# Optimization experiments

Measured on AMD Instinct MI355X. Metric: run time of the kernel, lower is better.

Reference implementation:

```python
import jax, jax.numpy as jnp
import numpy as np

WINDOW_SIZE = 7
NUM_HEADS = 6
DIM = 192
HEAD_DIM = DIM // NUM_HEADS


def _relative_position_index(ws: int) -> np.ndarray:
    coords = np.stack(np.meshgrid(np.arange(ws), np.arange(ws), indexing='ij'))  # [2, ws, ws]
    coords = coords.reshape(2, -1)  # [2, ws*ws]
    rel = coords[:, :, None] - coords[:, None, :]  # [2, N, N]
    rel = rel.transpose(1, 2, 0).astype(np.int64)  # [N, N, 2]
    rel[..., 0] += ws - 1
    rel[..., 1] += ws - 1
    rel[..., 0] *= 2 * ws - 1
    return rel.sum(-1)  # [N, N] in [0, (2*ws-1)^2)


def setup_inputs() -> dict:
    key = jax.random.key(0)
    ks = jax.random.split(key, 6)
    B, N, C = 8192, WINDOW_SIZE * WINDOW_SIZE, DIM
    return {
        'x': jax.random.normal(ks[0], (B, N, C), dtype=jnp.float32),
        'qkv_w': jax.random.normal(ks[1], (3 * C, C), dtype=jnp.float32) * 0.02,
        'qkv_b': jax.random.normal(ks[2], (3 * C,), dtype=jnp.float32) * 0.02,
        'proj_w': jax.random.normal(ks[3], (C, C), dtype=jnp.float32) * 0.02,
        'proj_b': jax.random.normal(ks[4], (C,), dtype=jnp.float32) * 0.02,
        'bias_table': jax.random.normal(ks[5], ((2 * WINDOW_SIZE - 1) ** 2, NUM_HEADS), dtype=jnp.float32) * 0.02,
    }


def reference(x, qkv_w, qkv_b, proj_w, proj_b, bias_table):
    B, N, C = x.shape
    H, hd = NUM_HEADS, HEAD_DIM
    scale = hd ** -0.5
    rel_idx = jnp.asarray(_relative_position_index(WINDOW_SIZE))  # [N, N] static

    qkv = x @ qkv_w.T + qkv_b  # [B, N, 3C]
    qkv = qkv.reshape(B, N, 3, H, hd).transpose(2, 0, 3, 1, 4)  # [3, B, H, N, hd]
    q, k, v = qkv[0], qkv[1], qkv[2]

    attn = jnp.einsum('bhnd,bhmd->bhnm', q * scale, k)  # [B, H, N, N]
    bias = bias_table[rel_idx]  # [N, N, H]
    attn = attn + bias.transpose(2, 0, 1)[None]  # broadcast over B
    attn = jax.nn.softmax(attn, axis=-1)

    out = jnp.einsum('bhnm,bhmd->bhnd', attn, v)  # [B, H, N, hd]
    out = out.transpose(0, 2, 1, 3).reshape(B, N, C)
    return out @ proj_w.T + proj_b
```

## Files before the change

kernel.cpp:

```cpp
#include <hip/hip_runtime.h>
#include <hip/hip_bf16.h>
#include <cstdint>
#include <cstddef>

typedef float  f32x4 __attribute__((ext_vector_type(4)));
typedef short  s16x8 __attribute__((ext_vector_type(8)));

#define NTOK   49
#define CDIM   192
#define HEADS  6
#define SCALE  0.17677669529663689f
#define LOG2E  1.4426950408889634f
#define SCL2   (0.17677669529663689f * 1.4426950408889634f)

#define WS_BIAS_BYTES  98304
#define WS_WQ_BYTES    221184
#define WS_TOTAL_BYTES (WS_BIAS_BYTES + WS_WQ_BYTES + 73728)

static __device__ __forceinline__ ushort f2bf(float f) {
  __hip_bfloat16 h = __float2bfloat16(f);
  union { __hip_bfloat16 h; ushort u; } c; c.h = h;
  return c.u;
}

static __device__ __forceinline__ s16x8 pack8(f32x4 a, f32x4 b) {
  union { s16x8 v; __hip_bfloat162 h[4]; } u;
  u.h[0] = __float22bfloat162_rn(make_float2(a[0], a[1]));
  u.h[1] = __float22bfloat162_rn(make_float2(a[2], a[3]));
  u.h[2] = __float22bfloat162_rn(make_float2(b[0], b[1]));
  u.h[3] = __float22bfloat162_rn(make_float2(b[2], b[3]));
  return u.v;
}

static __device__ __forceinline__ f32x4 mfma_bf16(s16x8 a, s16x8 b, f32x4 c) {
  return __builtin_amdgcn_mfma_f32_16x16x32_bf16(a, b, c, 0, 0, 0);
}

__global__ void wconv_kernel(const float* __restrict__ qkv_w,
                             const float* __restrict__ proj_w,
                             const float* __restrict__ bias_table,
                             ushort* __restrict__ wqs, ushort* __restrict__ wps,
                             float* __restrict__ biasT) {
  int i = blockIdx.x * 256 + threadIdx.x;
  if (i < 576 * 192) {
    int n = i / 192, k = i % 192;
    int dst = ((n >> 4) * 6 + (k >> 5)) * 512 + ((k >> 3) & 3) * 128 + (n & 15) * 8 + (k & 7);
    wqs[dst] = f2bf(qkv_w[i]);
  }
  if (i < 192 * 192) {
    int n = i / 192, k = i % 192;
    int dst = ((n >> 4) * 6 + (k >> 5)) * 512 + ((k >> 3) & 3) * 128 + (n & 15) * 8 + (k & 7);
    wps[dst] = f2bf(proj_w[i]);
  }
  if (i < HEADS * 4096) {
    int h = i >> 12, r = i & 4095;
    int lane = (r >> 2) & 63, e = r & 3;
    int qt = r >> 10, kt = (r >> 8) & 3;
    int q   = qt * 16 + (lane & 15);
    int key = kt * 16 + (lane >> 4) * 4 + e;
    float v;
    if (key >= NTOK)      v = -1e30f;
    else if (q >= NTOK)   v = 0.f;
    else {
      int qd = q / 7, qm = q % 7, kd = key / 7, km = key % 7;
      int ri = (qd - kd + 6) * 13 + (qm - km + 6);
      v = bias_table[ri * 6 + h] * LOG2E;
    }
    biasT[i] = v;
  }
}

template <bool WB>
__global__ __launch_bounds__(768, 3)
void wattn_kernel(const float* __restrict__ x,
                  const float* __restrict__ qkv_w, const float* __restrict__ qkv_b,
                  const float* __restrict__ proj_w, const float* __restrict__ proj_b,
                  const float* __restrict__ bias_table,
                  const ushort* __restrict__ wqs, const ushort* __restrict__ wps,
                  const float* __restrict__ biasT,
                  float* __restrict__ out, int nwin) {
  __shared__ __align__(16) ushort XB[2][64 * 200];
  __shared__ __align__(16) float  BL[WB ? 4 : 1024];

  const int tid  = threadIdx.x;
  const int lane = tid & 63;
  const int wv   = tid >> 6;
  const int winl = wv / 6;
  const int w    = wv - winl * 6;
  const int l16  = lane & 15;
  const int lk   = lane >> 4;
  const int win  = blockIdx.x * 2 + winl;
  const int h    = w;

#pragma unroll
  for (int it = 0; it < 8; ++it) {
    int v = tid + it * 768;
    int wl2 = v / 3072, r = v - wl2 * 3072;
    int row = r / 48, c4 = r - row * 48;
    int wgl = blockIdx.x * 2 + wl2;
    float4 f = {0.f, 0.f, 0.f, 0.f};
    if (row < NTOK && wgl < nwin)
      f = *(const float4*)(x + (size_t)wgl * (NTOK * CDIM) + row * CDIM + c4 * 4);
    union { ushort4 u; __hip_bfloat162 h[2]; } cc;
    cc.h[0] = __float22bfloat162_rn(make_float2(f.x, f.y));
    cc.h[1] = __float22bfloat162_rn(make_float2(f.z, f.w));
    *(ushort4*)&XB[wl2][row * 200 + c4 * 4] = cc.u;
  }
  if constexpr (!WB) {
    for (int v = tid; v < 169 * 6; v += 768) BL[v] = bias_table[v];
  }
  __syncthreads();

  s16x8 bq[4], ak[4], bv[2][2];

  {
    f32x4 qacc[2][4] = {};
    f32x4 kacc[2][4] = {};
#pragma unroll
    for (int ks = 0; ks < 6; ++ks) {
      const int k0 = ks * 32 + lk * 8;
      s16x8 xa[4];
#pragma unroll
      for (int mt = 0; mt < 4; ++mt)
        xa[mt] = *(const s16x8*)&XB[winl][(mt * 16 + l16) * 200 + k0];
#pragma unroll
      for (int nt2 = 0; nt2 < 2; ++nt2) {
        s16x8 wqf, wkf;
        if constexpr (WB) {
          const int lo = lk * 128 + l16 * 8;
          wqf = *(const s16x8*)&wqs[(((0 * 12 + w * 2 + nt2) * 6 + ks) << 9) + lo];
          wkf = *(const s16x8*)&wqs[(((1 * 12 + w * 2 + nt2) * 6 + ks) << 9) + lo];
        } else {
          const int nq = w * 32 + nt2 * 16 + l16;
          const float* p;
          p = qkv_w + (0 * 192 + nq) * 192 + k0;
          { float4 f0 = *(const float4*)p, f1 = *(const float4*)(p + 4);
            f32x4 a = {f0.x,f0.y,f0.z,f0.w}, b = {f1.x,f1.y,f1.z,f1.w}; wqf = pack8(a, b); }
          p = qkv_w + (1 * 192 + nq) * 192 + k0;
          { float4 f0 = *(const float4*)p, f1 = *(const float4*)(p + 4);
            f32x4 a = {f0.x,f0.y,f0.z,f0.w}, b = {f1.x,f1.y,f1.z,f1.w}; wkf = pack8(a, b); }
        }
#pragma unroll
        for (int mt = 0; mt < 4; ++mt) {
          qacc[nt2][mt] = mfma_bf16(wqf, xa[mt], qacc[nt2][mt]);
          kacc[nt2][mt] = mfma_bf16(wkf, xa[mt], kacc[nt2][mt]);
        }
      }
    }
    {
      const float4 b0 = *(const float4*)&qkv_b[0 * 192 + w * 32 +  0 + lk * 4];
      const float4 b1 = *(const float4*)&qkv_b[0 * 192 + w * 32 + 16 + lk * 4];
#pragma unroll
      for (int t = 0; t < 4; ++t) {
        f32x4 a0 = qacc[0][t], a1 = qacc[1][t];
        a0[0]=(a0[0]+b0.x)*SCL2; a0[1]=(a0[1]+b0.y)*SCL2; a0[2]=(a0[2]+b0.z)*SCL2; a0[3]=(a0[3]+b0.w)*SCL2;
        a1[0]=(a1[0]+b1.x)*SCL2; a1[1]=(a1[1]+b1.y)*SCL2; a1[2]=(a1[2]+b1.z)*SCL2; a1[3]=(a1[3]+b1.w)*SCL2;
        bq[t] = pack8(a0, a1);
      }
    }
#pragma unroll
    for (int t = 0; t < 4; ++t)
      ak[t] = pack8(kacc[0][t], kacc[1][t]);
  }

  {
    f32x4 vacc[4][2] = {};
#pragma unroll
    for (int ks = 0; ks < 6; ++ks) {
      const int k0 = ks * 32 + lk * 8;
      s16x8 xa[4];
#pragma unroll
      for (int mt = 0; mt < 4; ++mt)
        xa[mt] = *(const s16x8*)&XB[winl][(mt * 16 + l16) * 200 + k0];
#pragma unroll
      for (int nt2 = 0; nt2 < 2; ++nt2) {
        s16x8 wf;
        if constexpr (WB) {
          wf = *(const s16x8*)&wqs[(((2 * 12 + w * 2 + nt2) * 6 + ks) << 9) + lk * 128 + l16 * 8];
        } else {
          const float* p = qkv_w + (2 * 192 + w * 32 + nt2 * 16 + l16) * 192 + k0;
          float4 f0 = *(const float4*)p, f1 = *(const float4*)(p + 4);
          f32x4 a = {f0.x,f0.y,f0.z,f0.w}, b = {f1.x,f1.y,f1.z,f1.w}; wf = pack8(a, b);
        }
#pragma unroll
        for (int mt = 0; mt < 4; ++mt)
          vacc[mt][nt2] = mfma_bf16(xa[mt], wf, vacc[mt][nt2]);
      }
    }
#pragma unroll
    for (int nd = 0; nd < 2; ++nd) {
      const float vb = qkv_b[2 * 192 + w * 32 + nd * 16 + l16];
      f32x4 v0 = vacc[0][nd], v1 = vacc[1][nd], v2 = vacc[2][nd], v3 = vacc[3][nd];
#pragma unroll
      for (int i = 0; i < 4; ++i) { v0[i]+=vb; v1[i]+=vb; v2[i]+=vb; v3[i]+=vb; }
      bv[nd][0] = pack8(v0, v1);
      bv[nd][1] = pack8(v2, v3);
    }
  }
  __syncthreads();

#pragma unroll
  for (int qt = 0; qt < 4; ++qt) {
    f32x4 s[4];
#pragma unroll
    for (int kt = 0; kt < 4; ++kt) {
      f32x4 z = {0.f, 0.f, 0.f, 0.f};
      s[kt] = mfma_bf16(ak[kt], bq[qt], z);
    }
    float mx = -1e30f;
    if constexpr (WB) {
#pragma unroll
      for (int kt = 0; kt < 4; ++kt) {
        f32x4 b4 = *(const f32x4*)&biasT[h * 4096 + qt * 1024 + kt * 256 + lane * 4];
#pragma unroll
        for (int i = 0; i < 4; ++i) {
          float sv = s[kt][i] + b4[i];
          s[kt][i] = sv;
          mx = fmaxf(mx, sv);
        }
      }
    } else {
      const int q  = qt * 16 + l16;
      const int qd = q / 7, qm = q % 7;
#pragma unroll
      for (int kt = 0; kt < 4; ++kt)
#pragma unroll
        for (int i = 0; i < 4; ++i) {
          const int key = kt * 16 + lk * 4 + i;
          float sv = s[kt][i];
          if (key < NTOK) {
            int kd = key / 7, km = key % 7;
            int ri = (qd - kd + 6) * 13 + (qm - km + 6);
            ri = ri < 0 ? 0 : (ri > 168 ? 168 : ri);
            sv += BL[ri * 6 + h] * LOG2E;
          } else sv = -1e30f;
          s[kt][i] = sv;
          mx = fmaxf(mx, sv);
        }
    }
    mx = fmaxf(mx, __shfl_xor(mx, 16));
    mx = fmaxf(mx, __shfl_xor(mx, 32));
    float sum = 0.f;
#pragma unroll
    for (int kt = 0; kt < 4; ++kt)
#pragma unroll
      for (int i = 0; i < 4; ++i) {
        float p = exp2f(s[kt][i] - mx);
        s[kt][i] = p; sum += p;
      }
    sum += __shfl_xor(sum, 16);
    sum += __shfl_xor(sum, 32);
    const float rinv = 1.f / sum;
#pragma unroll
    for (int kt = 0; kt < 4; ++kt)
#pragma unroll
      for (int i = 0; i < 4; ++i) s[kt][i] *= rinv;

    s16x8 pa0 = pack8(s[0], s[1]);
    s16x8 pa1 = pack8(s[2], s[3]);
#pragma unroll
    for (int nd = 0; nd < 2; ++nd) {
      f32x4 z = {0.f, 0.f, 0.f, 0.f};
      f32x4 o = mfma_bf16(pa0, bv[nd][0], z);
      o = mfma_bf16(pa1, bv[nd][1], o);
#pragma unroll
      for (int i = 0; i < 4; ++i)
        XB[winl][(qt * 16 + lk * 4 + i) * 200 + h * 32 + nd * 16 + l16] = f2bf(o[i]);
    }
  }
  __syncthreads();

  {
    f32x4 pc[4][2] = {};
#pragma unroll
    for (int ks = 0; ks < 6; ++ks) {
      const int k0 = ks * 32 + lk * 8;
      s16x8 a[4];
#pragma unroll
      for (int mt = 0; mt < 4; ++mt)
        a[mt] = *(const s16x8*)&XB[winl][(mt * 16 + l16) * 200 + k0];
#pragma unroll
      for (int nt = 0; nt < 2; ++nt) {
        s16x8 b;
        if constexpr (WB) {
          b = *(const s16x8*)&wps[(((w * 2 + nt) * 6 + ks) << 9) + lk * 128 + l16 * 8];
        } else {
          const int n = w * 32 + nt * 16 + l16;
          const float* p = proj_w + n * 192 + k0;
          float4 f0 = *(const float4*)p, f1 = *(const float4*)(p + 4);
          f32x4 fa = {f0.x,f0.y,f0.z,f0.w}, fb = {f1.x,f1.y,f1.z,f1.w};
          b = pack8(fa, fb);
        }
#pragma unroll
        for (int mt = 0; mt < 4; ++mt)
          pc[mt][nt] = mfma_bf16(a[mt], b, pc[mt][nt]);
      }
    }
    if (win < nwin) {
#pragma unroll
      for (int nt = 0; nt < 2; ++nt) {
        const int n = w * 32 + nt * 16 + l16;
        const float pbias = proj_b[n];
#pragma unroll
        for (int mt = 0; mt < 4; ++mt)
#pragma unroll
          for (int i = 0; i < 4; ++i) {
            const int row = mt * 16 + lk * 4 + i;
            if (row < NTOK)
              out[((size_t)win * NTOK + row) * CDIM + n] = pc[mt][nt][i] + pbias;
          }
      }
    }
  }
}

extern "C" void kernel_launch(void* const* d_in, const int* in_sizes, int n_in,
                              void* d_out, int out_size, void* d_ws, size_t ws_size,
                              hipStream_t stream) {
  const float* x          = (const float*)d_in[0];
  const float* qkv_w      = (const float*)d_in[1];
  const float* qkv_b      = (const float*)d_in[2];
  const float* proj_w     = (const float*)d_in[3];
  const float* proj_b     = (const float*)d_in[4];
  const float* bias_table = (const float*)d_in[5];
  float* out = (float*)d_out;

  const int nwin = in_sizes[0] / (NTOK * CDIM);
  const int nblk = (nwin + 1) / 2;

  if (ws_size >= WS_TOTAL_BYTES) {
    float*  biasT = (float*)d_ws;
    ushort* wqs   = (ushort*)((char*)d_ws + WS_BIAS_BYTES);
    ushort* wps   = (ushort*)((char*)d_ws + WS_BIAS_BYTES + WS_WQ_BYTES);
    wconv_kernel<<<dim3(432), dim3(256), 0, stream>>>(qkv_w, proj_w, bias_table, wqs, wps, biasT);
    wattn_kernel<true><<<dim3(nblk), dim3(768), 0, stream>>>(
        x, qkv_w, qkv_b, proj_w, proj_b, bias_table, wqs, wps, biasT, out, nwin);
  } else {
    wattn_kernel<false><<<dim3(nblk), dim3(768), 0, stream>>>(
        x, qkv_w, qkv_b, proj_w, proj_b, bias_table, nullptr, nullptr, nullptr, out, nwin);
  }
}
```

Baseline: 409.0 us.

## Make attention blocks persistent over four window pairs with double-buffered x prefetch

Each block now processes four window pairs in a loop instead of one, using a double-buffered LDS region. The global loads of the next pair's x are issued into registers before the attention phase and written to the alternate buffer afterward, so load latency overlaps compute and launch count drops by four. In exchange it doubles LDS use per block (about 100KB), which may cut occupancy below the launch-bounds target, and adds register pressure from the staged float4s. Grid size shrinks, so tail and load-balance effects change.

```diff
diff --git a/kernel.cpp b/kernel.cpp
--- a/kernel.cpp
+++ b/kernel.cpp
@@ -12,6 +12,7 @@
 #define SCALE  0.17677669529663689f
 #define LOG2E  1.4426950408889634f
 #define SCL2   (0.17677669529663689f * 1.4426950408889634f)
+#define PPB    4
 
 #define WS_BIAS_BYTES  98304
 #define WS_WQ_BYTES    221184
@@ -21,6 +22,13 @@
   __hip_bfloat16 h = __float2bfloat16(f);
   union { __hip_bfloat16 h; ushort u; } c; c.h = h;
   return c.u;
+}
+
+static __device__ __forceinline__ ushort4 cvt4(float4 f) {
+  union { ushort4 u; __hip_bfloat162 h[2]; } cc;
+  cc.h[0] = __float22bfloat162_rn(make_float2(f.x, f.y));
+  cc.h[1] = __float22bfloat162_rn(make_float2(f.z, f.w));
+  return cc.u;
 }
 
 static __device__ __forceinline__ s16x8 pack8(f32x4 a, f32x4 b) {
@@ -79,7 +87,7 @@
                   const ushort* __restrict__ wqs, const ushort* __restrict__ wps,
                   const float* __restrict__ biasT,
                   float* __restrict__ out, int nwin) {
-  __shared__ __align__(16) ushort XB[2][64 * 200];
+  __shared__ __align__(16) ushort XB[2][2][64 * 200];
   __shared__ __align__(16) float  BL[WB ? 4 : 1024];
 
   const int tid  = threadIdx.x;
@@ -89,65 +97,66 @@
   const int w    = wv - winl * 6;
   const int l16  = lane & 15;
   const int lk   = lane >> 4;
-  const int win  = blockIdx.x * 2 + winl;
   const int h    = w;
+  const int pair0 = blockIdx.x * PPB;
 
 #pragma unroll
   for (int it = 0; it < 8; ++it) {
     int v = tid + it * 768;
     int wl2 = v / 3072, r = v - wl2 * 3072;
     int row = r / 48, c4 = r - row * 48;
-    int wgl = blockIdx.x * 2 + wl2;
+    int wgl = pair0 * 2 + wl2;
     float4 f = {0.f, 0.f, 0.f, 0.f};
     if (row < NTOK && wgl < nwin)
       f = *(const float4*)(x + (size_t)wgl * (NTOK * CDIM) + row * CDIM + c4 * 4);
-    union { ushort4 u; __hip_bfloat162 h[2]; } cc;
-    cc.h[0] = __float22bfloat162_rn(make_float2(f.x, f.y));
-    cc.h[1] = __float22bfloat162_rn(make_float2(f.z, f.w));
-    *(ushort4*)&XB[wl2][row * 200 + c4 * 4] = cc.u;
+    *(ushort4*)&XB[0][wl2][row * 200 + c4 * 4] = cvt4(f);
   }
   if constexpr (!WB) {
     for (int v = tid; v < 169 * 6; v += 768) BL[v] = bias_table[v];
   }
   __syncthreads();
 
-  s16x8 bq[4], ak[4], bv[2][2];
-
-  {
-    f32x4 qacc[2][4] = {};
-    f32x4 kacc[2][4] = {};
-#pragma unroll
-    for (int ks = 0; ks < 6; ++ks) {
-      const int k0 = ks * 32 + lk * 8;
-      s16x8 xa[4];
-#pragma unroll
-      for (int mt = 0; mt < 4; ++mt)
-        xa[mt] = *(const s16x8*)&XB[winl][(mt * 16 + l16) * 200 + k0];
-#pragma unroll
-      for (int nt2 = 0; nt2 < 2; ++nt2) {
-        s16x8 wqf, wkf;
-        if constexpr (WB) {
-          const int lo = lk * 128 + l16 * 8;
-          wqf = *(const s16x8*)&wqs[(((0 * 12 + w * 2 + nt2) * 6 + ks) << 9) + lo];
-          wkf = *(const s16x8*)&wqs[(((1 * 12 + w * 2 + nt2) * 6 + ks) << 9) + lo];
-        } else {
-          const int nq = w * 32 + nt2 * 16 + l16;
-          const float* p;
-          p = qkv_w + (0 * 192 + nq) * 192 + k0;
-          { float4 f0 = *(const float4*)p, f1 = *(const float4*)(p + 4);
-            f32x4 a = {f0.x,f0.y,f0.z,f0.w}, b = {f1.x,f1.y,f1.z,f1.w}; wqf = pack8(a, b); }
-          p = qkv_w + (1 * 192 + nq) * 192 + k0;
-          { float4 f0 = *(const float4*)p, f1 = *(const float4*)(p + 4);
-            f32x4 a = {f0.x,f0.y,f0.z,f0.w}, b = {f1.x,f1.y,f1.z,f1.w}; wkf = pack8(a, b); }
-        }
-#pragma unroll
-        for (int mt = 0; mt < 4; ++mt) {
-          qacc[nt2][mt] = mfma_bf16(wqf, xa[mt], qacc[nt2][mt]);
-          kacc[nt2][mt] = mfma_bf16(wkf, xa[mt], kacc[nt2][mt]);
-        }
-      }
-    }
+  for (int p = 0; p < PPB; ++p) {
+    const int par = p & 1;
+    const int win = (pair0 + p) * 2 + winl;
+    const ushort* xb = XB[par][winl];
+
+    s16x8 bq[4], ak[4], bv[2][2];
+
     {
+      f32x4 qacc[2][4] = {};
+      f32x4 kacc[2][4] = {};
+#pragma unroll
+      for (int ks = 0; ks < 6; ++ks) {
+        const int k0 = ks * 32 + lk * 8;
+        s16x8 xa[4];
+#pragma unroll
+        for (int mt = 0; mt < 4; ++mt)
+          xa[mt] = *(const s16x8*)&xb[(mt * 16 + l16) * 200 + k0];
+#pragma unroll
+        for (int nt2 = 0; nt2 < 2; ++nt2) {
+          s16x8 wqf, wkf;
+          if constexpr (WB) {
+            const int lo = lk * 128 + l16 * 8;
+            wqf = *(const s16x8*)&wqs[(((0 * 12 + w * 2 + nt2) * 6 + ks) << 9) + lo];
+            wkf = *(const s16x8*)&wqs[(((1 * 12 + w * 2 + nt2) * 6 + ks) << 9) + lo];
+          } else {
+            const int nq = w * 32 + nt2 * 16 + l16;
+            const float* pp;
+            pp = qkv_w + (0 * 192 + nq) * 192 + k0;
+            { float4 f0 = *(const float4*)pp, f1 = *(const float4*)(pp + 4);
+              f32x4 a = {f0.x,f0.y,f0.z,f0.w}, b = {f1.x,f1.y,f1.z,f1.w}; wqf = pack8(a, b); }
+            pp = qkv_w + (1 * 192 + nq) * 192 + k0;
+            { float4 f0 = *(const float4*)pp, f1 = *(const float4*)(pp + 4);
+              f32x4 a = {f0.x,f0.y,f0.z,f0.w}, b = {f1.x,f1.y,f1.z,f1.w}; wkf = pack8(a, b); }
+          }
+#pragma unroll
+          for (int mt = 0; mt < 4; ++mt) {
+            qacc[nt2][mt] = mfma_bf16(wqf, xa[mt], qacc[nt2][mt]);
+            kacc[nt2][mt] = mfma_bf16(wkf, xa[mt], kacc[nt2][mt]);
+          }
+        }
+      }
       const float4 b0 = *(const float4*)&qkv_b[0 * 192 + w * 32 +  0 + lk * 4];
       const float4 b1 = *(const float4*)&qkv_b[0 * 192 + w * 32 + 16 + lk * 4];
 #pragma unroll
@@ -157,158 +166,190 @@
         a1[0]=(a1[0]+b1.x)*SCL2; a1[1]=(a1[1]+b1.y)*SCL2; a1[2]=(a1[2]+b1.z)*SCL2; a1[3]=(a1[3]+b1.w)*SCL2;
         bq[t] = pack8(a0, a1);
       }
-    }
-#pragma unroll
-    for (int t = 0; t < 4; ++t)
-      ak[t] = pack8(kacc[0][t], kacc[1][t]);
-  }
-
-  {
-    f32x4 vacc[4][2] = {};
-#pragma unroll
-    for (int ks = 0; ks < 6; ++ks) {
-      const int k0 = ks * 32 + lk * 8;
-      s16x8 xa[4];
-#pragma unroll
-      for (int mt = 0; mt < 4; ++mt)
-        xa[mt] = *(const s16x8*)&XB[winl][(mt * 16 + l16) * 200 + k0];
-#pragma unroll
-      for (int nt2 = 0; nt2 < 2; ++nt2) {
-        s16x8 wf;
-        if constexpr (WB) {
-          wf = *(const s16x8*)&wqs[(((2 * 12 + w * 2 + nt2) * 6 + ks) << 9) + lk * 128 + l16 * 8];
-        } else {
-          const float* p = qkv_w + (2 * 192 + w * 32 + nt2 * 16 + l16) * 192 + k0;
-          float4 f0 = *(const float4*)p, f1 = *(const float4*)(p + 4);
-          f32x4 a = {f0.x,f0.y,f0.z,f0.w}, b = {f1.x,f1.y,f1.z,f1.w}; wf = pack8(a, b);
-        }
+#pragma unroll
+      for (int t = 0; t < 4; ++t)
+        ak[t] = pack8(kacc[0][t], kacc[1][t]);
+    }
+
+    {
+      f32x4 vacc[4][2] = {};
+#pragma unroll
+      for (int ks = 0; ks < 6; ++ks) {
+        const int k0 = ks * 32 + lk * 8;
+        s16x8 xa[4];
 #pragma unroll
         for (int mt = 0; mt < 4; ++mt)
-          vacc[mt][nt2] = mfma_bf16(xa[mt], wf, vacc[mt][nt2]);
-      }
-    }
-#pragma unroll
-    for (int nd = 0; nd < 2; ++nd) {
-      const float vb = qkv_b[2 * 192 + w * 32 + nd * 16 + l16];
-      f32x4 v0 = vacc[0][nd], v1 = vacc[1][nd], v2 = vacc[2][nd], v3 = vacc[3][nd];
-#pragma unroll
-      for (int i = 0; i < 4; ++i) { v0[i]+=vb; v1[i]+=vb; v2[i]+=vb; v3[i]+=vb; }
-      bv[nd][0] = pack8(v0, v1);
-      bv[nd][1] = pack8(v2, v3);
-    }
-  }
-  __syncthreads();
-
-#pragma unroll
-  for (int qt = 0; qt < 4; ++qt) {
-    f32x4 s[4];
-#pragma unroll
-    for (int kt = 0; kt < 4; ++kt) {
-      f32x4 z = {0.f, 0.f, 0.f, 0.f};
-      s[kt] = mfma_bf16(ak[kt], bq[qt], z);
-    }
-    float mx = -1e30f;
-    if constexpr (WB) {
+          xa[mt] = *(const s16x8*)&xb[(mt * 16 + l16) * 200 + k0];
+#pragma unroll
+        for (int nt2 = 0; nt2 < 2; ++nt2) {
+          s16x8 wf;
+          if constexpr (WB) {
+            wf = *(const s16x8*)&wqs[(((2 * 12 + w * 2 + nt2) * 6 + ks) << 9) + lk * 128 + l16 * 8];
+          } else {
+            const float* pp = qkv_w + (2 * 192 + w * 32 + nt2 * 16 + l16) * 192 + k0;
+            float4 f0 = *(const float4*)pp, f1 = *(const float4*)(pp + 4);
+            f32x4 a = {f0.x,f0.y,f0.z,f0.w}, b = {f1.x,f1.y,f1.z,f1.w}; wf = pack8(a, b);
+          }
+#pragma unroll
+          for (int mt = 0; mt < 4; ++mt)
+            vacc[mt][nt2] = mfma_bf16(xa[mt], wf, vacc[mt][nt2]);
+        }
+      }
+#pragma unroll
+      for (int nd = 0; nd < 2; ++nd) {
+        const float vb = qkv_b[2 * 192 + w * 32 + nd * 16 + l16];
+        f32x4 v0 = vacc[0][nd], v1 = vacc[1][nd], v2 = vacc[2][nd], v3 = vacc[3][nd];
+#pragma unroll
+        for (int i = 0; i < 4; ++i) { v0[i]+=vb; v1[i]+=vb; v2[i]+=vb; v3[i]+=vb; }
+        bv[nd][0] = pack8(v0, v1);
+        bv[nd][1] = pack8(v2, v3);
+      }
+    }
+
+    const bool do_stage = (p + 1 < PPB);
+    float4 st0, st1, st2, st3, st4, st5, st6, st7;
+    if (do_stage) {
+      const int np = pair0 + p + 1;
+#pragma unroll
+      for (int it = 0; it < 8; ++it) {
+        int v = tid + it * 768;
+        int wl2 = v / 3072, r = v - wl2 * 3072;
+        int row = r / 48, c4 = r - row * 48;
+        int wgl = np * 2 + wl2;
+        float4 f = {0.f, 0.f, 0.f, 0.f};
+        if (row < NTOK && wgl < nwin)
+          f = *(const float4*)(x + (size_t)wgl * (NTOK * CDIM) + row * CDIM + c4 * 4);
+        if (it == 0) st0 = f; else if (it == 1) st1 = f; else if (it == 2) st2 = f;
+        else if (it == 3) st3 = f; else if (it == 4) st4 = f; else if (it == 5) st5 = f;
+        else if (it == 6) st6 = f; else st7 = f;
+      }
+    }
+    __syncthreads();
+
+    ushort* xbw = XB[par][winl];
+#pragma unroll
+    for (int qt = 0; qt < 4; ++qt) {
+      f32x4 s[4];
 #pragma unroll
       for (int kt = 0; kt < 4; ++kt) {
-        f32x4 b4 = *(const f32x4*)&biasT[h * 4096 + qt * 1024 + kt * 256 + lane * 4];
+        f32x4 z = {0.f, 0.f, 0.f, 0.f};
+        s[kt] = mfma_bf16(ak[kt], bq[qt], z);
+      }
+      float mx = -1e30f;
+      if constexpr (WB) {
+#pragma unroll
+        for (int kt = 0; kt < 4; ++kt) {
+          f32x4 b4 = *(const f32x4*)&biasT[h * 4096 + qt * 1024 + kt * 256 + lane * 4];
+#pragma unroll
+          for (int i = 0; i < 4; ++i) {
+            float sv = s[kt][i] + b4[i];
+            s[kt][i] = sv;
+            mx = fmaxf(mx, sv);
+          }
+        }
+      } else {
+        const int q  = qt * 16 + l16;
+        const int qd = q / 7, qm = q % 7;
+#pragma unroll
+        for (int kt = 0; kt < 4; ++kt)
+#pragma unroll
+          for (int i = 0; i < 4; ++i) {
+            const int key = kt * 16 + lk * 4 + i;
+            float sv = s[kt][i];
+            if (key < NTOK) {
+              int kd = key / 7, km = key % 7;
+              int ri = (qd - kd + 6) * 13 + (qm - km + 6);
+              ri = ri < 0 ? 0 : (ri > 168 ? 168 : ri);
+              sv += BL[ri * 6 + h] * LOG2E;
+            } else sv = -1e30f;
+            s[kt][i] = sv;
+            mx = fmaxf(mx, sv);
+          }
+      }
+      mx = fmaxf(mx, __shfl_xor(mx, 16));
+      mx = fmaxf(mx, __shfl_xor(mx, 32));
+      float sum = 0.f;
+#pragma unroll
+      for (int kt = 0; kt < 4; ++kt)
 #pragma unroll
         for (int i = 0; i < 4; ++i) {
-          float sv = s[kt][i] + b4[i];
-          s[kt][i] = sv;
-          mx = fmaxf(mx, sv);
-        }
-      }
-    } else {
-      const int q  = qt * 16 + l16;
-      const int qd = q / 7, qm = q % 7;
+          float pv = exp2f(s[kt][i] - mx);
+          s[kt][i] = pv; sum += pv;
+        }
+      sum += __shfl_xor(sum, 16);
+      sum += __shfl_xor(sum, 32);
+      const float rinv = 1.f / sum;
 #pragma unroll
       for (int kt = 0; kt < 4; ++kt)
 #pragma unroll
-        for (int i = 0; i < 4; ++i) {
-          const int key = kt * 16 + lk * 4 + i;
-          float sv = s[kt][i];
-          if (key < NTOK) {
-            int kd = key / 7, km = key % 7;
-            int ri = (qd - kd + 6) * 13 + (qm - km + 6);
-            ri = ri < 0 ? 0 : (ri > 168 ? 168 : ri);
-            sv += BL[ri * 6 + h] * LOG2E;
-          } else sv = -1e30f;
-          s[kt][i] = sv;
-          mx = fmaxf(mx, sv);
-        }
-    }
-    mx = fmaxf(mx, __shfl_xor(mx, 16));
-    mx = fmaxf(mx, __shfl_xor(mx, 32));
-    float sum = 0.f;
-#pragma unroll
-    for (int kt = 0; kt < 4; ++kt)
-#pragma unroll
-      for (int i = 0; i < 4; ++i) {
-        float p = exp2f(s[kt][i] - mx);
-        s[kt][i] = p; sum += p;
-      }
-    sum += __shfl_xor(sum, 16);
-    sum += __shfl_xor(sum, 32);
-    const float rinv = 1.f / sum;
-#pragma unroll
-    for (int kt = 0; kt < 4; ++kt)
-#pragma unroll
-      for (int i = 0; i < 4; ++i) s[kt][i] *= rinv;
-
-    s16x8 pa0 = pack8(s[0], s[1]);
-    s16x8 pa1 = pack8(s[2], s[3]);
-#pragma unroll
-    for (int nd = 0; nd < 2; ++nd) {
-      f32x4 z = {0.f, 0.f, 0.f, 0.f};
-      f32x4 o = mfma_bf16(pa0, bv[nd][0], z);
-      o = mfma_bf16(pa1, bv[nd][1], o);
-#pragma unroll
-      for (int i = 0; i < 4; ++i)
-        XB[winl][(qt * 16 + lk * 4 + i) * 200 + h * 32 + nd * 16 + l16] = f2bf(o[i]);
-    }
-  }
-  __syncthreads();
-
-  {
-    f32x4 pc[4][2] = {};
-#pragma unroll
-    for (int ks = 0; ks < 6; ++ks) {
-      const int k0 = ks * 32 + lk * 8;
-      s16x8 a[4];
-#pragma unroll
-      for (int mt = 0; mt < 4; ++mt)
-        a[mt] = *(const s16x8*)&XB[winl][(mt * 16 + l16) * 200 + k0];
-#pragma unroll
-      for (int nt = 0; nt < 2; ++nt) {
-        s16x8 b;
-        if constexpr (WB) {
-          b = *(const s16x8*)&wps[(((w * 2 + nt) * 6 + ks) << 9) + lk * 128 + l16 * 8];
-        } else {
+        for (int i = 0; i < 4; ++i) s[kt][i] *= rinv;
+
+      s16x8 pa0 = pack8(s[0], s[1]);
+      s16x8 pa1 = pack8(s[2], s[3]);
+#pragma unroll
+      for (int nd = 0; nd < 2; ++nd) {
+        f32x4 z = {0.f, 0.f, 0.f, 0.f};
+        f32x4 o = mfma_bf16(pa0, bv[nd][0], z);
+        o = mfma_bf16(pa1, bv[nd][1], o);
+#pragma unroll
+        for (int i = 0; i < 4; ++i)
+          xbw[(qt * 16 + lk * 4 + i) * 200 + h * 32 + nd * 16 + l16] = f2bf(o[i]);
+      }
+    }
+
+    if (do_stage) {
+#pragma unroll
+      for (int it = 0; it < 8; ++it) {
+        int v = tid + it * 768;
+        int wl2 = v / 3072, r = v - wl2 * 3072;
+        int row = r / 48, c4 = r - row * 48;
+        float4 f = (it == 0) ? st0 : (it == 1) ? st1 : (it == 2) ? st2 : (it == 3) ? st3
+                 : (it == 4) ? st4 : (it == 5) ? st5 : (it == 6) ? st6 : st7;
+        *(ushort4*)&XB[par ^ 1][wl2][row * 200 + c4 * 4] = cvt4(f);
+      }
+    }
+    __syncthreads();
+
+    {
+      f32x4 pc[4][2] = {};
+#pragma unroll
+      for (int ks = 0; ks < 6; ++ks) {
+        const int k0 = ks * 32 + lk * 8;
+        s16x8 a[4];
+#pragma unroll
+        for (int mt = 0; mt < 4; ++mt)
+          a[mt] = *(const s16x8*)&xb[(mt * 16 + l16) * 200 + k0];
+#pragma unroll
+        for (int nt = 0; nt < 2; ++nt) {
+          s16x8 b;
+          if constexpr (WB) {
+            b = *(const s16x8*)&wps[(((w * 2 + nt) * 6 + ks) << 9) + lk * 128 + l16 * 8];
+          } else {
+            const int n = w * 32 + nt * 16 + l16;
+            const float* pp = proj_w + n * 192 + k0;
+            float4 f0 = *(const float4*)pp, f1 = *(const float4*)(pp + 4);
+            f32x4 fa = {f0.x,f0.y,f0.z,f0.w}, fb = {f1.x,f1.y,f1.z,f1.w};
+            b = pack8(fa, fb);
+          }
+#pragma unroll
+          for (int mt = 0; mt < 4; ++mt)
+            pc[mt][nt] = mfma_bf16(a[mt], b, pc[mt][nt]);
+        }
+      }
+      if (win < nwin) {
+#pragma unroll
+        for (int nt = 0; nt < 2; ++nt) {
           const int n = w * 32 + nt * 16 + l16;
-          const float* p = proj_w + n * 192 + k0;
-          float4 f0 = *(const float4*)p, f1 = *(const float4*)(p + 4);
-          f32x4 fa = {f0.x,f0.y,f0.z,f0.w}, fb = {f1.x,f1.y,f1.z,f1.w};
-          b = pack8(fa, fb);
-        }
-#pragma unroll
-        for (int mt = 0; mt < 4; ++mt)
-          pc[mt][nt] = mfma_bf16(a[mt], b, pc[mt][nt]);
-      }
-    }
-    if (win < nwin) {
-#pragma unroll
-      for (int nt = 0; nt < 2; ++nt) {
-        const int n = w * 32 + nt * 16 + l16;
-        const float pbias = proj_b[n];
-#pragma unroll
-        for (int mt = 0; mt < 4; ++mt)
-#pragma unroll
-          for (int i = 0; i < 4; ++i) {
-            const int row = mt * 16 + lk * 4 + i;
-            if (row < NTOK)
-              out[((size_t)win * NTOK + row) * CDIM + n] = pc[mt][nt][i] + pbias;
-          }
+          const float pbias = proj_b[n];
+#pragma unroll
+          for (int mt = 0; mt < 4; ++mt)
+#pragma unroll
+            for (int i = 0; i < 4; ++i) {
+              const int row = mt * 16 + lk * 4 + i;
+              if (row < NTOK)
+                out[((size_t)win * NTOK + row) * CDIM + n] = pc[mt][nt][i] + pbias;
+            }
+        }
       }
     }
   }
@@ -325,8 +366,9 @@
   const float* bias_table = (const float*)d_in[5];
   float* out = (float*)d_out;
 
-  const int nwin = in_sizes[0] / (NTOK * CDIM);
-  const int nblk = (nwin + 1) / 2;
+  const int nwin   = in_sizes[0] / (NTOK * CDIM);
+  const int npairs = (nwin + 1) / 2;
+  const int nblk   = (npairs + PPB - 1) / PPB;
 
   if (ws_size >= WS_TOTAL_BYTES) {
     float*  biasT = (float*)d_ws;
```

New measurement: 1.407 ms. 244% more time.
